# Performance work log

Measured on AMD Instinct MI355X. Metric: run time of the kernel, lower is better.

Reference implementation:

```python
import jax, jax.numpy as jnp
import numpy as np

N = 768          # number of proposals (graph nodes)
C = 1024         # box_head feature dim (in_feats)
HC = 256         # RelPN hidden_c
K = 20           # topk edges per node
GH = 256         # gcn_hidden
H1 = 4           # gat1 heads
IMG_H, IMG_W = 800.0, 800.0
NEG_SLOPE = 0.2  # PyG GATConv leaky_relu slope


def setup_inputs() -> dict:
    key = jax.random.key(0)
    ks = jax.random.split(key, 24)
    s = 0.02
    feats = jax.random.normal(ks[0], (N, C), jnp.float32)
    # valid boxes inside an 800x800 image
    cx = jax.random.uniform(ks[1], (N,), minval=100.0, maxval=700.0)
    cy = jax.random.uniform(ks[2], (N,), minval=100.0, maxval=700.0)
    w = jax.random.uniform(ks[3], (N,), minval=10.0, maxval=200.0)
    h = jax.random.uniform(ks[4], (N,), minval=10.0, maxval=200.0)
    boxes = jnp.stack([cx - 0.5 * w, cy - 0.5 * h, cx + 0.5 * w, cy + 0.5 * h], axis=1)
    rn = lambda k, sh: jax.random.normal(k, sh, jnp.float32) * s
    return {
        'feats': feats, 'boxes': boxes,
        # RelationProposalNetwork: fc1(2C+4 -> HC), fc2(HC -> 1)
        'W1': rn(ks[5], (2 * C + 4, HC)), 'b1': jnp.zeros((HC,), jnp.float32),
        'W2': rn(ks[6], (HC, 1)), 'b2': jnp.zeros((1,), jnp.float32),
        # GATConv(C+4 -> GH, heads=4)
        'g1W': rn(ks[7], (C + 4, H1 * GH)), 'g1as': rn(ks[8], (H1, GH)),
        'g1ad': rn(ks[9], (H1, GH)), 'g1b': jnp.zeros((H1 * GH,), jnp.float32),
        # GATConv(GH*4 -> 2, heads=1)
        'g2W': rn(ks[10], (H1 * GH, 2)), 'g2as': rn(ks[11], (1, 2)),
        'g2ad': rn(ks[12], (1, 2)), 'g2b': jnp.zeros((2,), jnp.float32),
        'rW1': rn(ks[13], (H1 * GH + 4, GH // 2)), 'rb1': jnp.zeros((GH // 2,), jnp.float32),
        'rW2': rn(ks[14], (GH // 2, 4)), 'rb2': jnp.zeros((4,), jnp.float32),
    }


def _gat(xin, W, a_src, a_dst, bias, heads, feat, nbr):
    """PyG-style GATConv (eval mode, self-loops already in nbr). nbr: [N, K+1] src ids per dst."""
    n = xin.shape[0]
    xp = (xin @ W).reshape(n, heads, feat)              # [N,H,F]
    asrc = jnp.einsum('nhf,hf->nh', xp, a_src)          # [N,H]
    adst = jnp.einsum('nhf,hf->nh', xp, a_dst)          # [N,H]
    logits = jax.nn.leaky_relu(asrc[nbr] + adst[:, None, :], NEG_SLOPE)  # [N,K+1,H]
    alpha = jax.nn.softmax(logits, axis=1)              # softmax over incoming edges per dst
    out = jnp.einsum('nkh,nkhf->nhf', alpha, xp[nbr])   # gather + weighted aggregate
    return out.reshape(n, heads * feat) + bias


def reference(feats, boxes, W1, b1, W2, b2, g1W, g1as, g1ad, g1b,
              g2W, g2as, g2ad, g2b, rW1, rb1, rW2, rb2):
    n = feats.shape[0]
    scale = jnp.array([IMG_W, IMG_H, IMG_W, IMG_H], jnp.float32)
    geom = boxes / scale                                 # _box_geom: normalized coords
    x = jnp.concatenate([feats, geom], axis=1)           # [N, C+4]

    # --- RelationProposalNetwork: fc1(cat[f_i, f_j, |b_i - b_j|]) decomposed ---
    Wa, Wb, Wg = W1[:C], W1[C:2 * C], W1[2 * C:]
    fa = feats @ Wa                                      # i-part  [N,HC]
    fb = feats @ Wb                                      # j-part  [N,HC]
    gdiff = jnp.abs(boxes[:, None, :] - boxes[None, :, :])          # [N,N,4]
    h = jax.nn.relu(fa[:, None, :] + fb[None, :, :]
                    + jnp.einsum('ijd,dh->ijh', gdiff, Wg) + b1)    # [N,N,HC]
    rel = jnp.einsum('ijh,h->ij', h, W2[:, 0]) + b2[0]              # [N,N]

    # --- top-k edges per destination node (exclude self), plus self-loops ---
    rel_masked = jnp.where(jnp.eye(n, dtype=bool), -1e9, rel)
    _, nbr = jax.lax.top_k(rel_masked, K)                # [N,K] src j for each dst i
    nbr = jnp.concatenate([nbr, jnp.arange(n)[:, None]], axis=1)    # [N,K+1]

    # --- GAT propagation ---
    h1 = jax.nn.relu(_gat(x, g1W, g1as, g1ad, g1b, H1, GH, nbr))    # [N,1024]
    logits = _gat(h1, g2W, g2as, g2ad, g2b, 1, 2, nbr)              # [N,2]

    reg_in = jnp.concatenate([h1, geom], axis=1)
    delta = jax.nn.relu(reg_in @ rW1 + rb1) @ rW2 + rb2             # [N,4]
    px0, py0, px1, py1 = boxes[:, 0], boxes[:, 1], boxes[:, 2], boxes[:, 3]
    pw, ph = px1 - px0, py1 - py0
    pcx, pcy = px0 + 0.5 * pw, py0 + 0.5 * ph
    dx, dy, dw, dh = delta[:, 0], delta[:, 1], delta[:, 2], delta[:, 3]
    gcx, gcy = dx * pw + pcx, dy * ph + pcy
    gw, gh = jnp.exp(dw) * pw, jnp.exp(dh) * ph
    final_boxes = jnp.stack([gcx - 0.5 * gw, gcy - 0.5 * gh,
                             gcx + 0.5 * gw, gcy + 0.5 * gh], axis=1)
    return jnp.concatenate([logits, final_boxes], axis=1)  # [N,6]
```

## Files before the change

### kernel.cpp

```cpp
#include <hip/hip_runtime.h>
#include <math.h>

#define NN 768
#define KK_TOP 20
#define NBR_K 21

typedef __attribute__((ext_vector_type(8))) short bf16x8;
typedef __attribute__((ext_vector_type(4))) float f32x4;
typedef unsigned short ushort_t;
typedef unsigned int uint_t;

__device__ __forceinline__ ushort_t f2bf(float x) {
    union { float f; uint_t u; } c; c.f = x;
    uint_t r = (c.u + 0x7FFFu + ((c.u >> 16) & 1u)) >> 16;
    return (ushort_t)r;
}
__device__ __forceinline__ float bf2f(ushort_t u) {
    union { uint_t u; float f; } c; c.u = ((uint_t)u) << 16;
    return c.f;
}

struct Params {
    const float *feats, *boxes, *W1, *b1, *W2, *b2;
    const float *g1W, *g1as, *g1ad, *g1b, *g2W, *g2as, *g2ad, *g2b;
    const float *rW1, *rb1, *rW2, *rb2;
    float *out;
    float *fafb, *xp, *relm, *hid, *Arow, *Brow, *asrc, *adst, *xp2, *aux2;
    float4 *wgt4; float *w2p, *consts;
    float *va, *vb, *av;
    int *nbr;
    ushort_t *featsbf, *btAB, *btG, *btR, *h1bf;
};

__global__ __launch_bounds__(256) void k_prep(Params P)
{
    int b = blockIdx.x, t = threadIdx.x;
    if (b == 800) {
        const float* Wg = P.W1 + 2048 * 256;
        float q0 = Wg[t], q1 = Wg[256 + t], q2 = Wg[512 + t], q3 = Wg[768 + t];
        float w2 = P.W2[t];
        P.wgt4[t] = make_float4(q0, q1, q2, q3);
        P.w2p[t] = w2;
        __shared__ float red[256];
        float vals[5] = {q0 * w2, q1 * w2, q2 * w2, q3 * w2, P.b1[t] * w2};
        for (int d = 0; d < 5; d++) {
            red[t] = vals[d]; __syncthreads();
            for (int s = 128; s > 0; s >>= 1) {
                if (t < s) red[t] += red[t + s];
                __syncthreads();
            }
            if (t == 0) P.consts[d] = red[0];
            __syncthreads();
        }
        return;
    }
    if (b >= 809) {
        int o = (b - 809) * 256 + t;
        if (o >= 8224) return;
        int vec = o / 1028, k = o - vec * 1028;
        int h = vec & 3;
        const float* aw = ((vec < 4) ? P.g1as : P.g1ad) + h * 256;
        const float* gw = P.g1W + (size_t)k * 1024 + h * 256;
        float s = 0.f;
        for (int f = 0; f < 256; f++) s += gw[f] * aw[f];
        P.av[vec * 1028 + k] = s;
        return;
    }
    if (b >= 801) {
        int o = (b - 801) * 256 + t;
        const float* row = P.W1 + (size_t)o * 256;
        float s = 0.f;
        for (int h = 0; h < 256; h++) s += row[h] * P.W2[h];
        if (o < 1024) P.va[o] = s; else P.vb[o - 1024] = s;
        return;
    }
    if (b >= 416) {
        int gid = (b - 416) * 2048 + t * 8;
        float4 v0 = *(const float4*)(P.feats + gid);
        float4 v1 = *(const float4*)(P.feats + gid + 4);
        uint4 r;
        r.x = (uint_t)f2bf(v0.x) | ((uint_t)f2bf(v0.y) << 16);
        r.y = (uint_t)f2bf(v0.z) | ((uint_t)f2bf(v0.w) << 16);
        r.z = (uint_t)f2bf(v1.x) | ((uint_t)f2bf(v1.y) << 16);
        r.w = (uint_t)f2bf(v1.z) | ((uint_t)f2bf(v1.w) << 16);
        *(uint4*)(P.featsbf + gid) = r;
        return;
    }
    const float* in; ushort_t* out; int ldN, tk, tn;
    if (b < 64)       { in = P.W1;              out = P.btAB;              ldN = 256;  tn = b & 3;  tk = b >> 2; }
    else if (b < 128) { int i = b - 64;  in = P.W1 + 1024 * 256; out = P.btAB + 256 * 1024; ldN = 256;  tn = i & 3;  tk = i >> 2; }
    else if (b < 384) { int i = b - 128; in = P.g1W;             out = P.btG;               ldN = 1024; tn = i & 15; tk = i >> 4; }
    else              { int i = b - 384; in = P.rW1;             out = P.btR;               ldN = 128;  tn = i & 1;  tk = i >> 1; }

    __shared__ __align__(16) float tile[64][68];
    int k0 = tk * 64, n0 = tn * 64;
#pragma unroll
    for (int it = 0; it < 4; it++) {
        int r = (t >> 4) + it * 16;
        int c = (t & 15) * 4;
        *(float4*)&tile[r][c] = *(const float4*)(in + (size_t)(k0 + r) * ldN + n0 + c);
    }
    __syncthreads();
    int n = t >> 2;
    int kc = (t & 3) * 16;
    uint_t p[8];
#pragma unroll
    for (int h = 0; h < 8; h++) {
        ushort_t lo = f2bf(tile[kc + 2 * h][n]);
        ushort_t hi = f2bf(tile[kc + 2 * h + 1][n]);
        p[h] = (uint_t)lo | ((uint_t)hi << 16);
    }
    ushort_t* dst = out + (size_t)(n0 + n) * 1024 + k0 + kc;
    *(uint4*)dst = make_uint4(p[0], p[1], p[2], p[3]);
    *(uint4*)(dst + 8) = make_uint4(p[4], p[5], p[6], p[7]);
}

__device__ __forceinline__ void mfma_unit(
    int bx, int by, const ushort_t* __restrict__ A, const ushort_t* __restrict__ Bt,
    float* __restrict__ C, int ldc, int mode,
    const float* __restrict__ boxes, const float* __restrict__ Wgeo,
    const float* __restrict__ bias, int t, char* smem)
{
    ushort_t (*As)[72] = (ushort_t(*)[72])smem;
    ushort_t (*Bs)[72] = (ushort_t(*)[72])(smem + 64 * 72 * 2);
    int m0 = by * 64, n0 = bx * 64;
    int lane = t & 63, w = t >> 6;
    int quad = lane >> 4, ci = lane & 15;

    int r0 = t >> 3, q0 = t & 7;
    int r1 = (t + 256) >> 3, q1 = (t + 256) & 7;

    const ushort_t* Abase = A + (size_t)(m0 + r0) * 1024 + q0 * 8;
    const ushort_t* Abase1 = A + (size_t)(m0 + r1) * 1024 + q1 * 8;
    const ushort_t* Bbase = Bt + (size_t)(n0 + r0) * 1024 + q0 * 8;
    const ushort_t* Bbase1 = Bt + (size_t)(n0 + r1) * 1024 + q1 * 8;

    uint4 pa0 = *(const uint4*)(Abase);
    uint4 pa1 = *(const uint4*)(Abase1);
    uint4 pb0 = *(const uint4*)(Bbase);
    uint4 pb1 = *(const uint4*)(Bbase1);

    f32x4 acc[2][2];
    acc[0][0] = (f32x4){0.f, 0.f, 0.f, 0.f};
    acc[0][1] = (f32x4){0.f, 0.f, 0.f, 0.f};
    acc[1][0] = (f32x4){0.f, 0.f, 0.f, 0.f};
    acc[1][1] = (f32x4){0.f, 0.f, 0.f, 0.f};

    int arow = (w & 1) * 32 + ci;
    int brow = (w >> 1) * 32 + ci;

    for (int kt = 0; kt < 16; kt++) {
        *(uint4*)&As[r0][q0 * 8] = pa0;
        *(uint4*)&As[r1][q1 * 8] = pa1;
        *(uint4*)&Bs[r0][q0 * 8] = pb0;
        *(uint4*)&Bs[r1][q1 * 8] = pb1;
        __syncthreads();
        if (kt < 15) {
            int ko = (kt + 1) * 64;
            pa0 = *(const uint4*)(Abase + ko);
            pa1 = *(const uint4*)(Abase1 + ko);
            pb0 = *(const uint4*)(Bbase + ko);
            pb1 = *(const uint4*)(Bbase1 + ko);
        }
#pragma unroll
        for (int s = 0; s < 2; s++) {
            int kb = s * 32 + quad * 8;
            bf16x8 a0 = *(const bf16x8*)&As[arow][kb];
            bf16x8 a1 = *(const bf16x8*)&As[arow + 16][kb];
            bf16x8 b0 = *(const bf16x8*)&Bs[brow][kb];
            bf16x8 b1 = *(const bf16x8*)&Bs[brow + 16][kb];
            acc[0][0] = __builtin_amdgcn_mfma_f32_16x16x32_bf16(a0, b0, acc[0][0], 0, 0, 0);
            acc[0][1] = __builtin_amdgcn_mfma_f32_16x16x32_bf16(a0, b1, acc[0][1], 0, 0, 0);
            acc[1][0] = __builtin_amdgcn_mfma_f32_16x16x32_bf16(a1, b0, acc[1][0], 0, 0, 0);
            acc[1][1] = __builtin_amdgcn_mfma_f32_16x16x32_bf16(a1, b1, acc[1][1], 0, 0, 0);
        }
        __syncthreads();
    }

    const float inv800 = 1.0f / 800.0f;
#pragma unroll
    for (int ni = 0; ni < 2; ni++) {
        int col = n0 + (w >> 1) * 32 + ni * 16 + ci;
        float wg0 = 0.f, wg1 = 0.f, wg2 = 0.f, wg3 = 0.f, bv = 0.f;
        if (mode) {
            wg0 = Wgeo[col]; wg1 = Wgeo[ldc + col];
            wg2 = Wgeo[2 * ldc + col]; wg3 = Wgeo[3 * ldc + col];
            if (mode == 2) bv = bias[col];
        }
#pragma unroll
        for (int mi = 0; mi < 2; mi++) {
            int rbase = m0 + (w & 1) * 32 + mi * 16 + quad * 4;
#pragma unroll
            for (int reg = 0; reg < 4; reg++) {
                int row = rbase + reg;
                float v = acc[mi][ni][reg];
                if (mode) {
                    float4 bx4 = *(const float4*)(boxes + row * 4);
                    v += (bx4.x * wg0 + bx4.y * wg1 + bx4.z * wg2 + bx4.w * wg3) * inv800 + bv;
                    if (mode == 2) v = fmaxf(v, 0.f);
                }
                C[(size_t)row * ldc + col] = v;
            }
        }
    }
}

__global__ __launch_bounds__(256) void k_gemms(Params P)
{
    __shared__ __align__(16) char smem[18432];
    int u = blockIdx.x, t = threadIdx.x;
    if (u < 96) {
        mfma_unit(u & 7, u >> 3, P.featsbf, P.btAB, P.fafb, 512, 0,
                  nullptr, nullptr, nullptr, t, smem);
    } else if (u < 288) {
        int v = u - 96;
        mfma_unit(v & 15, v >> 4, P.featsbf, P.btG, P.xp, 1024, 1,
                  P.boxes, P.g1W + (size_t)1024 * 1024, nullptr, t, smem);
    } else if (u < 480) {
        int row = (u - 288) * 4 + (t >> 6);
        int lane = t & 63;
        const float4* fr = (const float4*)(P.feats + (size_t)row * 1024);
        const float4* va4 = (const float4*)P.va;
        const float4* vb4 = (const float4*)P.vb;
        float s1 = 0.f, s2 = 0.f;
#pragma unroll
        for (int it = 0; it < 4; it++) {
            int idx = it * 64 + lane;
            float4 f = fr[idx], a = va4[idx], b = vb4[idx];
            s1 += f.x * a.x + f.y * a.y + f.z * a.z + f.w * a.w;
            s2 += f.x * b.x + f.y * b.y + f.z * b.z + f.w * b.w;
        }
#pragma unroll
        for (int off = 32; off > 0; off >>= 1) {
            s1 += __shfl_xor(s1, off);
            s2 += __shfl_xor(s2, off);
        }
        if (lane == 0) { P.Arow[row] = s1; P.Brow[row] = s2; }
    } else {
        int pair = (u - 480) * 4 + (t >> 6);
        int lane = t & 63;
        int n = pair >> 2, h = pair & 3;
        const float4* fr = (const float4*)(P.feats + (size_t)n * 1024);
        const float* vs = P.av + h * 1028;
        const float* vd = P.av + (4 + h) * 1028;
        const float4* vs4 = (const float4*)vs;
        const float4* vd4 = (const float4*)vd;
        float s1 = 0.f, s2 = 0.f;
#pragma unroll
        for (int it = 0; it < 4; it++) {
            int idx = it * 64 + lane;
            float4 f = fr[idx], a = vs4[idx], b = vd4[idx];
            s1 += f.x * a.x + f.y * a.y + f.z * a.z + f.w * a.w;
            s2 += f.x * b.x + f.y * b.y + f.z * b.z + f.w * b.w;
        }
#pragma unroll
        for (int off = 32; off > 0; off >>= 1) {
            s1 += __shfl_xor(s1, off);
            s2 += __shfl_xor(s2, off);
        }
        if (lane == 0) {
            const float inv800 = 1.0f / 800.0f;
            float4 bx = *(const float4*)(P.boxes + n * 4);
            float g0 = bx.x * inv800, g1 = bx.y * inv800, g2 = bx.z * inv800, g3 = bx.w * inv800;
            s1 += g0 * vs[1024] + g1 * vs[1025] + g2 * vs[1026] + g3 * vs[1027];
            s2 += g0 * vd[1024] + g1 * vd[1025] + g2 * vd[1026] + g3 * vd[1027];
            P.asrc[n * 4 + h] = s1;
            P.adst[n * 4 + h] = s2;
        }
    }
}

#define REL_ACC(FA0, FA1, FB0, FB1, Q, W)                                           \
    {                                                                               \
        float v;                                                                    \
        v = FA0 + FB0;                                                              \
        v = fmaf(g00.x, Q.x, v); v = fmaf(g00.y, Q.y, v);                           \
        v = fmaf(g00.z, Q.z, v); v = fmaf(g00.w, Q.w, v);                           \
        acc00 = fmaf(fabsf(v), W, acc00);                                           \
        v = FA0 + FB1;                                                              \
        v = fmaf(g01.x, Q.x, v); v = fmaf(g01.y, Q.y, v);                           \
        v = fmaf(g01.z, Q.z, v); v = fmaf(g01.w, Q.w, v);                           \
        acc01 = fmaf(fabsf(v), W, acc01);                                           \
        v = FA1 + FB0;                                                              \
        v = fmaf(g10.x, Q.x, v); v = fmaf(g10.y, Q.y, v);                           \
        v = fmaf(g10.z, Q.z, v); v = fmaf(g10.w, Q.w, v);                           \
        acc10 = fmaf(fabsf(v), W, acc10);                                           \
        v = FA1 + FB1;                                                              \
        v = fmaf(g11.x, Q.x, v); v = fmaf(g11.y, Q.y, v);                           \
        v = fmaf(g11.z, Q.z, v); v = fmaf(g11.w, Q.w, v);                           \
        acc11 = fmaf(fabsf(v), W, acc11);                                           \
    }

__global__ __launch_bounds__(256) void k_rel(Params P)
{
    __shared__ __align__(16) float fas[32][68];
    __shared__ __align__(16) float fbs[32][68];
    int t = threadIdx.x;
    int bx = blockIdx.x % 24, by = blockIdx.x / 24;
    int tx = t & 15, ty = t >> 4;
    int i0 = by * 32, j0 = bx * 32;
    int ia = i0 + ty, ib = i0 + ty + 16;
    int ja = j0 + tx, jb = j0 + tx + 16;

    float4 Bi0 = *(const float4*)(P.boxes + ia * 4);
    float4 Bi1 = *(const float4*)(P.boxes + ib * 4);
    float4 Bj0 = *(const float4*)(P.boxes + ja * 4);
    float4 Bj1 = *(const float4*)(P.boxes + jb * 4);
    float4 g00 = make_float4(fabsf(Bi0.x - Bj0.x), fabsf(Bi0.y - Bj0.y), fabsf(Bi0.z - Bj0.z), fabsf(Bi0.w - Bj0.w));
    float4 g01 = make_float4(fabsf(Bi0.x - Bj1.x), fabsf(Bi0.y - Bj1.y), fabsf(Bi0.z - Bj1.z), fabsf(Bi0.w - Bj1.w));
    float4 g10 = make_float4(fabsf(Bi1.x - Bj0.x), fabsf(Bi1.y - Bj0.y), fabsf(Bi1.z - Bj0.z), fabsf(Bi1.w - Bj0.w));
    float4 g11 = make_float4(fabsf(Bi1.x - Bj1.x), fabsf(Bi1.y - Bj1.y), fabsf(Bi1.z - Bj1.z), fabsf(Bi1.w - Bj1.w));

    float acc00 = 0.f, acc01 = 0.f, acc10 = 0.f, acc11 = 0.f;

    for (int p = 0; p < 4; p++) {
        for (int e = t; e < 512; e += 256) {
            int r = e >> 4, cq = e & 15;
            float4 bb = *(const float4*)(P.b1 + p * 64 + cq * 4);
            float4 fv = *(const float4*)(P.fafb + (size_t)(i0 + r) * 512 + p * 64 + cq * 4);
            float4 gv = *(const float4*)(P.fafb + (size_t)(j0 + r) * 512 + 256 + p * 64 + cq * 4);
            *(float4*)&fas[r][cq * 4] = make_float4(fv.x + bb.x, fv.y + bb.y, fv.z + bb.z, fv.w + bb.w);
            *(float4*)&fbs[r][cq * 4] = gv;
        }
        __syncthreads();
        const float4* wg = P.wgt4 + p * 64;
        const float* w2 = P.w2p + p * 64;
#pragma unroll 8
        for (int hc = 0; hc < 16; hc++) {
            int h4 = hc * 4;
            float4 fa0 = *(const float4*)&fas[ty][h4];
            float4 fa1 = *(const float4*)&fas[ty + 16][h4];
            float4 fb0 = *(const float4*)&fbs[tx][h4];
            float4 fb1 = *(const float4*)&fbs[tx + 16][h4];
            float4 w2v = *(const float4*)(w2 + h4);
            float4 q0 = wg[h4], q1 = wg[h4 + 1], q2 = wg[h4 + 2], q3 = wg[h4 + 3];
            REL_ACC(fa0.x, fa1.x, fb0.x, fb1.x, q0, w2v.x);
            REL_ACC(fa0.y, fa1.y, fb0.y, fb1.y, q1, w2v.y);
            REL_ACC(fa0.z, fa1.z, fb0.z, fb1.z, q2, w2v.z);
            REL_ACC(fa0.w, fa1.w, fb0.w, fb1.w, q3, w2v.w);
        }
        __syncthreads();
    }

    float c0 = P.consts[0], c1 = P.consts[1], c2 = P.consts[2], c3 = P.consts[3], c4 = P.consts[4];
    float b2v = P.b2[0];
    float Ai0 = P.Arow[ia], Ai1 = P.Arow[ib];
    float Bja = P.Brow[ja], Bjb = P.Brow[jb];

    float lin, r00, r01, r10, r11;
    lin = Ai0 + Bja + g00.x * c0 + g00.y * c1 + g00.z * c2 + g00.w * c3 + c4;
    r00 = 0.5f * (lin + acc00) + b2v;
    lin = Ai0 + Bjb + g01.x * c0 + g01.y * c1 + g01.z * c2 + g01.w * c3 + c4;
    r01 = 0.5f * (lin + acc01) + b2v;
    lin = Ai1 + Bja + g10.x * c0 + g10.y * c1 + g10.z * c2 + g10.w * c3 + c4;
    r10 = 0.5f * (lin + acc10) + b2v;
    lin = Ai1 + Bjb + g11.x * c0 + g11.y * c1 + g11.z * c2 + g11.w * c3 + c4;
    r11 = 0.5f * (lin + acc11) + b2v;
    P.relm[(size_t)ia * NN + ja] = (ia == ja) ? -1e9f : r00;
    P.relm[(size_t)ia * NN + jb] = (ia == jb) ? -1e9f : r01;
    P.relm[(size_t)ib * NN + ja] = (ib == ja) ? -1e9f : r10;
    P.relm[(size_t)ib * NN + jb] = (ib == jb) ? -1e9f : r11;
}

__global__ __launch_bounds__(256) void k_topkgat1(Params P)
{
    int n = blockIdx.x, t = threadIdx.x;
    __shared__ int nb[NBR_K];
    __shared__ float alpha[NBR_K][4];

    if (t < 64) {
        int lane = t;
        const float* rp = P.relm + (size_t)n * NN;
        float v[12];
#pragma unroll
        for (int q = 0; q < 12; q++) v[q] = rp[q * 64 + lane];
        for (int kk = 0; kk < KK_TOP; kk++) {
            float best = v[0]; int bq = 0;
#pragma unroll
            for (int q = 1; q < 12; q++) {
                if (v[q] > best) { best = v[q]; bq = q; }
            }
            int bidx = bq * 64 + lane;
#pragma unroll
            for (int off = 32; off > 0; off >>= 1) {
                float ov = __shfl_xor(best, off);
                int oi = __shfl_xor(bidx, off);
                if (ov > best || (ov == best && oi < bidx)) { best = ov; bidx = oi; }
            }
            if (lane == 0) { nb[kk] = bidx; P.nbr[n * NBR_K + kk] = bidx; }
            int bl = bidx & 63, bq2 = bidx >> 6;
            if (lane == bl) {
#pragma unroll
                for (int q = 0; q < 12; q++)
                    if (q == bq2) v[q] = -INFINITY;
            }
        }
        if (lane == 0) { nb[KK_TOP] = n; P.nbr[n * NBR_K + KK_TOP] = n; }
    }
    __syncthreads();

    if (t < NBR_K * 4) {
        int k = t % NBR_K, h = t / NBR_K;
        float e = P.asrc[nb[k] * 4 + h] + P.adst[n * 4 + h];
        e = (e > 0.f) ? e : 0.2f * e;
        alpha[k][h] = e;
    }
    __syncthreads();
    if (t < 4) {
        float m = -INFINITY;
        for (int k = 0; k < NBR_K; k++) m = fmaxf(m, alpha[k][t]);
        float s = 0.f;
        for (int k = 0; k < NBR_K; k++) { float ex = expf(alpha[k][t] - m); alpha[k][t] = ex; s += ex; }
        float inv = 1.f / s;
        for (int k = 0; k < NBR_K; k++) alpha[k][t] *= inv;
    }
    __syncthreads();
#pragma unroll
    for (int q = 0; q < 4; q++) {
        int c = q * 256 + t;
        int h = c >> 8;
        float acc = 0.f;
        for (int k = 0; k < NBR_K; k++) acc += alpha[k][h] * P.xp[(size_t)nb[k] * 1024 + c];
        P.h1bf[(size_t)n * 1024 + c] = f2bf(fmaxf(acc + P.g1b[c], 0.f));
    }
}

__global__ __launch_bounds__(256) void k_p6(Params P)
{
    __shared__ __align__(16) char smem[18432];
    int u = blockIdx.x, t = threadIdx.x;
    if (u < 192) {
        int wid = u * 4 + (t >> 6);
        int lane = t & 63;
        float s0 = 0.f, s1 = 0.f;
#pragma unroll
        for (int it = 0; it < 4; it++) {
            int k = it * 256 + lane * 4;
            uint2 pk = *(const uint2*)(P.h1bf + (size_t)wid * 1024 + k);
            float v0 = bf2f((ushort_t)(pk.x & 0xFFFF));
            float v1 = bf2f((ushort_t)(pk.x >> 16));
            float v2 = bf2f((ushort_t)(pk.y & 0xFFFF));
            float v3 = bf2f((ushort_t)(pk.y >> 16));
            float4 w0 = *(const float4*)(P.g2W + k * 2);
            float4 w1 = *(const float4*)(P.g2W + k * 2 + 4);
            s0 += v0 * w0.x + v1 * w0.z + v2 * w1.x + v3 * w1.z;
            s1 += v0 * w0.y + v1 * w0.w + v2 * w1.y + v3 * w1.w;
        }
#pragma unroll
        for (int off = 32; off > 0; off >>= 1) { s0 += __shfl_down(s0, off); s1 += __shfl_down(s1, off); }
        if (lane == 0) {
            P.xp2[wid * 2 + 0] = s0; P.xp2[wid * 2 + 1] = s1;
            P.aux2[wid * 2 + 0] = s0 * P.g2as[0] + s1 * P.g2as[1];
            P.aux2[wid * 2 + 1] = s0 * P.g2ad[0] + s1 * P.g2ad[1];
        }
    } else {
        int v = u - 192;
        mfma_unit(v & 1, v >> 1, P.h1bf, P.btR, P.hid, 128, 2,
                  P.boxes, P.rW1 + (size_t)1024 * 128, P.rb1, t, smem);
    }
}

__global__ __launch_bounds__(256) void k_p7(Params P)
{
    int u = blockIdx.x, t = threadIdx.x;
    if (u < 3) {
        int n = u * 256 + t;
        float adstv = P.aux2[n * 2 + 1];
        int nb[NBR_K];
        float e[NBR_K];
        float m = -INFINITY;
        for (int k = 0; k < NBR_K; k++) {
            nb[k] = P.nbr[n * NBR_K + k];
            float v = P.aux2[nb[k] * 2 + 0] + adstv;
            v = (v > 0.f) ? v : 0.2f * v;
            e[k] = v; m = fmaxf(m, v);
        }
        float s = 0.f;
        for (int k = 0; k < NBR_K; k++) { e[k] = expf(e[k] - m); s += e[k]; }
        float inv = 1.f / s;
        float o0 = 0.f, o1 = 0.f;
        for (int k = 0; k < NBR_K; k++) {
            float a = e[k] * inv;
            o0 += a * P.xp2[nb[k] * 2 + 0];
            o1 += a * P.xp2[nb[k] * 2 + 1];
        }
        P.out[n * 6 + 0] = o0 + P.g2b[0];
        P.out[n * 6 + 1] = o1 + P.g2b[1];
    } else {
        int n = (u - 3) * 256 + t;
        float d0 = 0.f, d1 = 0.f, d2 = 0.f, d3 = 0.f;
        for (int k = 0; k < 128; k++) {
            float v = P.hid[n * 128 + k];
            d0 += v * P.rW2[k * 4 + 0];
            d1 += v * P.rW2[k * 4 + 1];
            d2 += v * P.rW2[k * 4 + 2];
            d3 += v * P.rW2[k * 4 + 3];
        }
        d0 += P.rb2[0]; d1 += P.rb2[1]; d2 += P.rb2[2]; d3 += P.rb2[3];
        float x0 = P.boxes[n * 4 + 0], y0 = P.boxes[n * 4 + 1];
        float x1 = P.boxes[n * 4 + 2], y1 = P.boxes[n * 4 + 3];
        float pw = x1 - x0, ph = y1 - y0;
        float pcx = x0 + 0.5f * pw, pcy = y0 + 0.5f * ph;
        float gcx = d0 * pw + pcx, gcy = d1 * ph + pcy;
        float gw = expf(d2) * pw, gh = expf(d3) * ph;
        P.out[n * 6 + 2] = gcx - 0.5f * gw;
        P.out[n * 6 + 3] = gcy - 0.5f * gh;
        P.out[n * 6 + 4] = gcx + 0.5f * gw;
        P.out[n * 6 + 5] = gcy + 0.5f * gh;
    }
}

extern "C" void kernel_launch(void* const* d_in, const int* in_sizes, int n_in,
                              void* d_out, int out_size, void* d_ws, size_t ws_size,
                              hipStream_t stream)
{
    Params P;
    P.feats = (const float*)d_in[0];
    P.boxes = (const float*)d_in[1];
    P.W1    = (const float*)d_in[2];
    P.b1    = (const float*)d_in[3];
    P.W2    = (const float*)d_in[4];
    P.b2    = (const float*)d_in[5];
    P.g1W   = (const float*)d_in[6];
    P.g1as  = (const float*)d_in[7];
    P.g1ad  = (const float*)d_in[8];
    P.g1b   = (const float*)d_in[9];
    P.g2W   = (const float*)d_in[10];
    P.g2as  = (const float*)d_in[11];
    P.g2ad  = (const float*)d_in[12];
    P.g2b   = (const float*)d_in[13];
    P.rW1   = (const float*)d_in[14];
    P.rb1   = (const float*)d_in[15];
    P.rW2   = (const float*)d_in[16];
    P.rb2   = (const float*)d_in[17];
    P.out   = (float*)d_out;

    float* ws = (float*)d_ws;
    P.fafb  = ws;
    P.xp    = P.fafb + 393216;
    P.relm  = P.xp + 786432;
    P.hid   = P.relm + 589824;
    P.Arow  = P.hid + 98304;
    P.Brow  = P.Arow + 768;
    P.asrc  = P.Brow + 768;
    P.adst  = P.asrc + 3072;
    P.xp2   = P.adst + 3072;
    P.aux2  = P.xp2 + 1536;
    P.wgt4  = (float4*)(P.aux2 + 1536);
    P.w2p   = (float*)(P.wgt4 + 256);
    P.consts= P.w2p + 256;
    P.va    = P.consts + 8;
    P.vb    = P.va + 1024;
    P.av    = P.vb + 1024;
    P.nbr   = (int*)(P.av + 8224);
    P.featsbf = (ushort_t*)(P.nbr + 16128);
    P.btAB    = P.featsbf + 786432;
    P.btG     = P.btAB + 524288;
    P.btR     = P.btG + 1048576;
    P.h1bf    = P.btR + 131072;

    k_prep    <<<dim3(842),  dim3(256), 0, stream>>>(P);
    k_gemms   <<<dim3(1248), dim3(256), 0, stream>>>(P);
    k_rel     <<<dim3(576),  dim3(256), 0, stream>>>(P);
    k_topkgat1<<<dim3(768),  dim3(256), 0, stream>>>(P);
    k_p6      <<<dim3(216),  dim3(256), 0, stream>>>(P);
    k_p7      <<<dim3(6),    dim3(256), 0, stream>>>(P);
}
```

Before: 207.3 us.

## Fuse regressor and final GAT into one kernel, warp-parallelize prep dot products

The per-thread serial dot products in k_prep become wave-per-output float4 loads with shuffle reductions, which raises the prep grid size. k_rel now stages its small weight vectors in shared memory. The GAT1 aggregation uses vectorized float4 gathers. k_p6 and k_p7 are merged into k_final: a 64x128 MFMA regressor tile keeps the hidden activations in shared memory and applies rW2 and the box decode in place, and the last block to finish (detected with an atomic counter) runs the GAT2 softmax. This removes one launch and the hid round trip through global memory, at the cost of a serialized last-block tail and a counter that must be reset on every call.

```diff
diff --git a/kernel.cpp b/kernel.cpp
--- a/kernel.cpp
+++ b/kernel.cpp
@@ -25,9 +25,10 @@
     const float *g1W, *g1as, *g1ad, *g1b, *g2W, *g2as, *g2ad, *g2b;
     const float *rW1, *rb1, *rW2, *rb2;
     float *out;
-    float *fafb, *xp, *relm, *hid, *Arow, *Brow, *asrc, *adst, *xp2, *aux2;
+    float *fafb, *xp, *relm, *Arow, *Brow, *asrc, *adst, *xp2, *aux2;
     float4 *wgt4; float *w2p, *consts;
     float *va, *vb, *av;
+    int *counter;
     int *nbr;
     ushort_t *featsbf, *btAB, *btG, *btR, *h1bf;
 };
@@ -41,6 +42,7 @@
         float w2 = P.W2[t];
         P.wgt4[t] = make_float4(q0, q1, q2, q3);
         P.w2p[t] = w2;
+        if (t == 0) P.counter[0] = 0;
         __shared__ float red[256];
         float vals[5] = {q0 * w2, q1 * w2, q2 * w2, q3 * w2, P.b1[t] * w2};
         for (int d = 0; d < 5; d++) {
@@ -54,24 +56,31 @@
         }
         return;
     }
-    if (b >= 809) {
-        int o = (b - 809) * 256 + t;
+    if (b >= 1313) {
+        int o = (b - 1313) * 4 + (t >> 6);
+        int lane = t & 63;
         if (o >= 8224) return;
         int vec = o / 1028, k = o - vec * 1028;
         int h = vec & 3;
-        const float* aw = ((vec < 4) ? P.g1as : P.g1ad) + h * 256;
-        const float* gw = P.g1W + (size_t)k * 1024 + h * 256;
-        float s = 0.f;
-        for (int f = 0; f < 256; f++) s += gw[f] * aw[f];
-        P.av[vec * 1028 + k] = s;
+        const float4* aw = (const float4*)(((vec < 4) ? P.g1as : P.g1ad) + h * 256);
+        const float4* gw = (const float4*)(P.g1W + (size_t)k * 1024 + h * 256);
+        float4 a = aw[lane], g = gw[lane];
+        float s = a.x * g.x + a.y * g.y + a.z * g.z + a.w * g.w;
+#pragma unroll
+        for (int off = 32; off > 0; off >>= 1) s += __shfl_xor(s, off);
+        if (lane == 0) P.av[o] = s;
         return;
     }
     if (b >= 801) {
-        int o = (b - 801) * 256 + t;
-        const float* row = P.W1 + (size_t)o * 256;
-        float s = 0.f;
-        for (int h = 0; h < 256; h++) s += row[h] * P.W2[h];
-        if (o < 1024) P.va[o] = s; else P.vb[o - 1024] = s;
+        int o = (b - 801) * 4 + (t >> 6);
+        int lane = t & 63;
+        const float4* row = (const float4*)(P.W1 + (size_t)o * 256);
+        float4 w = ((const float4*)P.W2)[lane];
+        float4 f = row[lane];
+        float s = f.x * w.x + f.y * w.y + f.z * w.z + f.w * w.w;
+#pragma unroll
+        for (int off = 32; off > 0; off >>= 1) s += __shfl_xor(s, off);
+        if (lane == 0) { if (o < 1024) P.va[o] = s; else P.vb[o - 1024] = s; }
         return;
     }
     if (b >= 416) {
@@ -119,7 +128,7 @@
     int bx, int by, const ushort_t* __restrict__ A, const ushort_t* __restrict__ Bt,
     float* __restrict__ C, int ldc, int mode,
     const float* __restrict__ boxes, const float* __restrict__ Wgeo,
-    const float* __restrict__ bias, int t, char* smem)
+    int t, char* smem)
 {
     ushort_t (*As)[72] = (ushort_t(*)[72])smem;
     ushort_t (*Bs)[72] = (ushort_t(*)[72])(smem + 64 * 72 * 2);
@@ -181,11 +190,10 @@
 #pragma unroll
     for (int ni = 0; ni < 2; ni++) {
         int col = n0 + (w >> 1) * 32 + ni * 16 + ci;
-        float wg0 = 0.f, wg1 = 0.f, wg2 = 0.f, wg3 = 0.f, bv = 0.f;
+        float wg0 = 0.f, wg1 = 0.f, wg2 = 0.f, wg3 = 0.f;
         if (mode) {
             wg0 = Wgeo[col]; wg1 = Wgeo[ldc + col];
             wg2 = Wgeo[2 * ldc + col]; wg3 = Wgeo[3 * ldc + col];
-            if (mode == 2) bv = bias[col];
         }
 #pragma unroll
         for (int mi = 0; mi < 2; mi++) {
@@ -196,8 +204,7 @@
                 float v = acc[mi][ni][reg];
                 if (mode) {
                     float4 bx4 = *(const float4*)(boxes + row * 4);
-                    v += (bx4.x * wg0 + bx4.y * wg1 + bx4.z * wg2 + bx4.w * wg3) * inv800 + bv;
-                    if (mode == 2) v = fmaxf(v, 0.f);
+                    v += (bx4.x * wg0 + bx4.y * wg1 + bx4.z * wg2 + bx4.w * wg3) * inv800;
                 }
                 C[(size_t)row * ldc + col] = v;
             }
@@ -211,11 +218,11 @@
     int u = blockIdx.x, t = threadIdx.x;
     if (u < 96) {
         mfma_unit(u & 7, u >> 3, P.featsbf, P.btAB, P.fafb, 512, 0,
-                  nullptr, nullptr, nullptr, t, smem);
+                  nullptr, nullptr, t, smem);
     } else if (u < 288) {
         int v = u - 96;
         mfma_unit(v & 15, v >> 4, P.featsbf, P.btG, P.xp, 1024, 1,
-                  P.boxes, P.g1W + (size_t)1024 * 1024, nullptr, t, smem);
+                  P.boxes, P.g1W + (size_t)1024 * 1024, t, smem);
     } else if (u < 480) {
         int row = (u - 288) * 4 + (t >> 6);
         int lane = t & 63;
@@ -295,12 +302,17 @@
 {
     __shared__ __align__(16) float fas[32][68];
     __shared__ __align__(16) float fbs[32][68];
+    __shared__ __align__(16) float4 wgt_s[256];
+    __shared__ __align__(16) float w2_s[256];
     int t = threadIdx.x;
     int bx = blockIdx.x % 24, by = blockIdx.x / 24;
     int tx = t & 15, ty = t >> 4;
     int i0 = by * 32, j0 = bx * 32;
     int ia = i0 + ty, ib = i0 + ty + 16;
     int ja = j0 + tx, jb = j0 + tx + 16;
+
+    wgt_s[t] = P.wgt4[t];
+    w2_s[t] = P.w2p[t];
 
     float4 Bi0 = *(const float4*)(P.boxes + ia * 4);
     float4 Bi1 = *(const float4*)(P.boxes + ib * 4);
@@ -323,8 +335,8 @@
             *(float4*)&fbs[r][cq * 4] = gv;
         }
         __syncthreads();
-        const float4* wg = P.wgt4 + p * 64;
-        const float* w2 = P.w2p + p * 64;
+        const float4* wg = wgt_s + p * 64;
+        const float* w2 = w2_s + p * 64;
 #pragma unroll 8
         for (int hc = 0; hc < 16; hc++) {
             int h4 = hc * 4;
@@ -415,20 +427,29 @@
         for (int k = 0; k < NBR_K; k++) alpha[k][t] *= inv;
     }
     __syncthreads();
-#pragma unroll
-    for (int q = 0; q < 4; q++) {
-        int c = q * 256 + t;
-        int h = c >> 8;
-        float acc = 0.f;
-        for (int k = 0; k < NBR_K; k++) acc += alpha[k][h] * P.xp[(size_t)nb[k] * 1024 + c];
-        P.h1bf[(size_t)n * 1024 + c] = f2bf(fmaxf(acc + P.g1b[c], 0.f));
-    }
-}
-
-__global__ __launch_bounds__(256) void k_p6(Params P)
+
+    int h = t >> 6;
+    float ax = 0.f, ay = 0.f, az = 0.f, aw = 0.f;
+#pragma unroll 7
+    for (int k = 0; k < NBR_K; k++) {
+        float a = alpha[k][h];
+        float4 xv = ((const float4*)(P.xp + (size_t)nb[k] * 1024))[t];
+        ax = fmaf(a, xv.x, ax); ay = fmaf(a, xv.y, ay);
+        az = fmaf(a, xv.z, az); aw = fmaf(a, xv.w, aw);
+    }
+    float4 gb = ((const float4*)P.g1b)[t];
+    uint2 pk;
+    pk.x = (uint_t)f2bf(fmaxf(ax + gb.x, 0.f)) | ((uint_t)f2bf(fmaxf(ay + gb.y, 0.f)) << 16);
+    pk.y = (uint_t)f2bf(fmaxf(az + gb.z, 0.f)) | ((uint_t)f2bf(fmaxf(aw + gb.w, 0.f)) << 16);
+    *(uint2*)(P.h1bf + (size_t)n * 1024 + t * 4) = pk;
+}
+
+__global__ __launch_bounds__(256) void k_final(Params P)
 {
-    __shared__ __align__(16) char smem[18432];
+    __shared__ __align__(16) char smem[33792];
+    __shared__ int lastFlag;
     int u = blockIdx.x, t = threadIdx.x;
+
     if (u < 192) {
         int wid = u * 4 + (t >> 6);
         int lane = t & 63;
@@ -455,58 +476,149 @@
         }
     } else {
         int v = u - 192;
-        mfma_unit(v & 1, v >> 1, P.h1bf, P.btR, P.hid, 128, 2,
-                  P.boxes, P.rW1 + (size_t)1024 * 128, P.rb1, t, smem);
-    }
-}
-
-__global__ __launch_bounds__(256) void k_p7(Params P)
-{
-    int u = blockIdx.x, t = threadIdx.x;
-    if (u < 3) {
-        int n = u * 256 + t;
-        float adstv = P.aux2[n * 2 + 1];
-        int nb[NBR_K];
-        float e[NBR_K];
-        float m = -INFINITY;
-        for (int k = 0; k < NBR_K; k++) {
-            nb[k] = P.nbr[n * NBR_K + k];
-            float v = P.aux2[nb[k] * 2 + 0] + adstv;
-            v = (v > 0.f) ? v : 0.2f * v;
-            e[k] = v; m = fmaxf(m, v);
-        }
+        int m0 = v * 64;
+        int lane = t & 63, w = t >> 6;
+        int quad = lane >> 4, ci = lane & 15;
+        ushort_t (*As)[72] = (ushort_t(*)[72])smem;
+        ushort_t (*Bs)[72] = (ushort_t(*)[72])(smem + 64 * 72 * 2);
+
+        int ra[2], qa[2], rb[4], qb[4];
+        const ushort_t* Ab[2]; const ushort_t* Bb[4];
+#pragma unroll
+        for (int i = 0; i < 2; i++) {
+            int c = t + 256 * i;
+            ra[i] = c >> 3; qa[i] = c & 7;
+            Ab[i] = P.h1bf + (size_t)(m0 + ra[i]) * 1024 + qa[i] * 8;
+        }
+#pragma unroll
+        for (int i = 0; i < 4; i++) {
+            int c = t + 256 * i;
+            rb[i] = c >> 3; qb[i] = c & 7;
+            Bb[i] = P.btR + (size_t)rb[i] * 1024 + qb[i] * 8;
+        }
+        uint4 pa[2], pb[4];
+#pragma unroll
+        for (int i = 0; i < 2; i++) pa[i] = *(const uint4*)(Ab[i]);
+#pragma unroll
+        for (int i = 0; i < 4; i++) pb[i] = *(const uint4*)(Bb[i]);
+
+        f32x4 acc[2][4];
+#pragma unroll
+        for (int mi = 0; mi < 2; mi++)
+#pragma unroll
+            for (int nf = 0; nf < 4; nf++) acc[mi][nf] = (f32x4){0.f, 0.f, 0.f, 0.f};
+
+        int arow = (w & 1) * 32 + ci;
+        int colbase = (w >> 1) * 64;
+
+        for (int kt = 0; kt < 16; kt++) {
+#pragma unroll
+            for (int i = 0; i < 2; i++) *(uint4*)&As[ra[i]][qa[i] * 8] = pa[i];
+#pragma unroll
+            for (int i = 0; i < 4; i++) *(uint4*)&Bs[rb[i]][qb[i] * 8] = pb[i];
+            __syncthreads();
+            if (kt < 15) {
+                int ko = (kt + 1) * 64;
+#pragma unroll
+                for (int i = 0; i < 2; i++) pa[i] = *(const uint4*)(Ab[i] + ko);
+#pragma unroll
+                for (int i = 0; i < 4; i++) pb[i] = *(const uint4*)(Bb[i] + ko);
+            }
+#pragma unroll
+            for (int s = 0; s < 2; s++) {
+                int kb = s * 32 + quad * 8;
+                bf16x8 a0 = *(const bf16x8*)&As[arow][kb];
+                bf16x8 a1 = *(const bf16x8*)&As[arow + 16][kb];
+#pragma unroll
+                for (int nf = 0; nf < 4; nf++) {
+                    bf16x8 bv = *(const bf16x8*)&Bs[colbase + nf * 16 + ci][kb];
+                    acc[0][nf] = __builtin_amdgcn_mfma_f32_16x16x32_bf16(a0, bv, acc[0][nf], 0, 0, 0);
+                    acc[1][nf] = __builtin_amdgcn_mfma_f32_16x16x32_bf16(a1, bv, acc[1][nf], 0, 0, 0);
+                }
+            }
+            __syncthreads();
+        }
+
+        float (*hid_s)[132] = (float(*)[132])smem;
+        const float* Wgeo = P.rW1 + 1024 * 128;
+        const float inv800 = 1.0f / 800.0f;
+        __syncthreads();
+#pragma unroll
+        for (int nf = 0; nf < 4; nf++) {
+            int col = colbase + nf * 16 + ci;
+            float wg0 = Wgeo[col], wg1 = Wgeo[128 + col];
+            float wg2 = Wgeo[256 + col], wg3 = Wgeo[384 + col];
+            float bv = P.rb1[col];
+#pragma unroll
+            for (int mi = 0; mi < 2; mi++) {
+                int rbase = (w & 1) * 32 + mi * 16 + quad * 4;
+#pragma unroll
+                for (int reg = 0; reg < 4; reg++) {
+                    int rl = rbase + reg;
+                    float4 bx4 = *(const float4*)(P.boxes + (m0 + rl) * 4);
+                    float val = acc[mi][nf][reg]
+                        + (bx4.x * wg0 + bx4.y * wg1 + bx4.z * wg2 + bx4.w * wg3) * inv800 + bv;
+                    hid_s[rl][col] = fmaxf(val, 0.f);
+                }
+            }
+        }
+        __syncthreads();
+
+        int r = t >> 2, d = t & 3;
         float s = 0.f;
-        for (int k = 0; k < NBR_K; k++) { e[k] = expf(e[k] - m); s += e[k]; }
-        float inv = 1.f / s;
-        float o0 = 0.f, o1 = 0.f;
-        for (int k = 0; k < NBR_K; k++) {
-            float a = e[k] * inv;
-            o0 += a * P.xp2[nb[k] * 2 + 0];
-            o1 += a * P.xp2[nb[k] * 2 + 1];
-        }
-        P.out[n * 6 + 0] = o0 + P.g2b[0];
-        P.out[n * 6 + 1] = o1 + P.g2b[1];
-    } else {
-        int n = (u - 3) * 256 + t;
-        float d0 = 0.f, d1 = 0.f, d2 = 0.f, d3 = 0.f;
-        for (int k = 0; k < 128; k++) {
-            float v = P.hid[n * 128 + k];
-            d0 += v * P.rW2[k * 4 + 0];
-            d1 += v * P.rW2[k * 4 + 1];
-            d2 += v * P.rW2[k * 4 + 2];
-            d3 += v * P.rW2[k * 4 + 3];
-        }
-        d0 += P.rb2[0]; d1 += P.rb2[1]; d2 += P.rb2[2]; d3 += P.rb2[3];
-        float x0 = P.boxes[n * 4 + 0], y0 = P.boxes[n * 4 + 1];
-        float x1 = P.boxes[n * 4 + 2], y1 = P.boxes[n * 4 + 3];
-        float pw = x1 - x0, ph = y1 - y0;
-        float pcx = x0 + 0.5f * pw, pcy = y0 + 0.5f * ph;
-        float gcx = d0 * pw + pcx, gcy = d1 * ph + pcy;
-        float gw = expf(d2) * pw, gh = expf(d3) * ph;
-        P.out[n * 6 + 2] = gcx - 0.5f * gw;
-        P.out[n * 6 + 3] = gcy - 0.5f * gh;
-        P.out[n * 6 + 4] = gcx + 0.5f * gw;
-        P.out[n * 6 + 5] = gcy + 0.5f * gh;
+        const float* hrow = &hid_s[r][0];
+        for (int k = 0; k < 128; k++) s = fmaf(hrow[k], P.rW2[k * 4 + d], s);
+        float s1v = __shfl_down(s, 1);
+        float s2v = __shfl_down(s, 2);
+        float s3v = __shfl_down(s, 3);
+        if (d == 0) {
+            int row = m0 + r;
+            float d0 = s + P.rb2[0], d1 = s1v + P.rb2[1];
+            float d2 = s2v + P.rb2[2], d3 = s3v + P.rb2[3];
+            float4 bx = *(const float4*)(P.boxes + row * 4);
+            float pw = bx.z - bx.x, ph = bx.w - bx.y;
+            float pcx = bx.x + 0.5f * pw, pcy = bx.y + 0.5f * ph;
+            float gcx = d0 * pw + pcx, gcy = d1 * ph + pcy;
+            float gw = expf(d2) * pw, gh = expf(d3) * ph;
+            P.out[row * 6 + 2] = gcx - 0.5f * gw;
+            P.out[row * 6 + 3] = gcy - 0.5f * gh;
+            P.out[row * 6 + 4] = gcx + 0.5f * gw;
+            P.out[row * 6 + 5] = gcy + 0.5f * gh;
+        }
+    }
+
+    __syncthreads();
+    if (t == 0) {
+        __threadfence();
+        int old = atomicAdd(P.counter, 1);
+        lastFlag = (old == 203) ? 1 : 0;
+    }
+    __syncthreads();
+    if (lastFlag) {
+        __threadfence();
+        for (int n = t; n < NN; n += 256) {
+            float adstv = P.aux2[n * 2 + 1];
+            int nbk[NBR_K];
+            float e[NBR_K];
+            float m = -INFINITY;
+            for (int k = 0; k < NBR_K; k++) {
+                nbk[k] = P.nbr[n * NBR_K + k];
+                float vv = P.aux2[nbk[k] * 2 + 0] + adstv;
+                vv = (vv > 0.f) ? vv : 0.2f * vv;
+                e[k] = vv; m = fmaxf(m, vv);
+            }
+            float ssum = 0.f;
+            for (int k = 0; k < NBR_K; k++) { e[k] = expf(e[k] - m); ssum += e[k]; }
+            float inv = 1.f / ssum;
+            float o0 = 0.f, o1 = 0.f;
+            for (int k = 0; k < NBR_K; k++) {
+                float a = e[k] * inv;
+                o0 += a * P.xp2[nbk[k] * 2 + 0];
+                o1 += a * P.xp2[nbk[k] * 2 + 1];
+            }
+            P.out[n * 6 + 0] = o0 + P.g2b[0];
+            P.out[n * 6 + 1] = o1 + P.g2b[1];
+        }
     }
 }
 
@@ -539,8 +651,7 @@
     P.fafb  = ws;
     P.xp    = P.fafb + 393216;
     P.relm  = P.xp + 786432;
-    P.hid   = P.relm + 589824;
-    P.Arow  = P.hid + 98304;
+    P.Arow  = P.relm + 589824;
     P.Brow  = P.Arow + 768;
     P.asrc  = P.Brow + 768;
     P.adst  = P.asrc + 3072;
@@ -552,17 +663,17 @@
     P.va    = P.consts + 8;
     P.vb    = P.va + 1024;
     P.av    = P.vb + 1024;
-    P.nbr   = (int*)(P.av + 8224);
+    P.counter = (int*)(P.av + 8224);
+    P.nbr   = P.counter + 8;
     P.featsbf = (ushort_t*)(P.nbr + 16128);
     P.btAB    = P.featsbf + 786432;
     P.btG     = P.btAB + 524288;
     P.btR     = P.btG + 1048576;
     P.h1bf    = P.btR + 131072;
 
-    k_prep    <<<dim3(842),  dim3(256), 0, stream>>>(P);
+    k_prep    <<<dim3(3369), dim3(256), 0, stream>>>(P);
     k_gemms   <<<dim3(1248), dim3(256), 0, stream>>>(P);
     k_rel     <<<dim3(576),  dim3(256), 0, stream>>>(P);
     k_topkgat1<<<dim3(768),  dim3(256), 0, stream>>>(P);
-    k_p6      <<<dim3(216),  dim3(256), 0, stream>>>(P);
-    k_p7      <<<dim3(6),    dim3(256), 0, stream>>>(P);
-}
+    k_final   <<<dim3(204),  dim3(256), 0, stream>>>(P);
+}
```

Result: slower. 238.8 us (+15.2%).
